# Kernel tuning notes

Hardware: AMD Instinct MI355X
Metric: run time of the kernel (lower is better)

## Reference

```python
import jax, jax.numpy as jnp
import numpy as np

D, H, NL, DFF, VS, VT = 512, 8, 6, 2048, 32000, 32000
B, SS, ST = 4, 512, 512
PAD = 1
EPS = 1e-5


def _pos_encoding(S, d):
    pos = jnp.arange(S, dtype=jnp.float32)[:, None]
    div = jnp.exp(jnp.arange(0, d, 2, dtype=jnp.float32) * (-jnp.log(jnp.float32(10000.0)) / d))
    pe = jnp.zeros((S, d), dtype=jnp.float32)
    pe = pe.at[:, 0::2].set(jnp.sin(pos * div))
    pe = pe.at[:, 1::2].set(jnp.cos(pos * div))
    return pe


def _ln(x, g, b):
    m = jnp.mean(x, axis=-1, keepdims=True)
    v = jnp.mean(jnp.square(x - m), axis=-1, keepdims=True)
    return (x - m) * jax.lax.rsqrt(v + EPS) * g + b


def _mha(q, k, v, Wq, Wk, Wv, Wo, mask):
    # q,k,v: [B,S,D]; W*: [D,D] (torch Linear: y = x @ W.T); mask True -> masked
    Bq, Sq, _ = q.shape
    Sk = k.shape[1]
    dk = D // H
    Q = (q @ Wq.T).reshape(Bq, Sq, H, dk).transpose(0, 2, 1, 3)
    K = (k @ Wk.T).reshape(Bq, Sk, H, dk).transpose(0, 2, 1, 3)
    V = (v @ Wv.T).reshape(Bq, Sk, H, dk).transpose(0, 2, 1, 3)
    scores = jnp.einsum('bhqd,bhkd->bhqk', Q, K) / jnp.sqrt(jnp.float32(dk))
    scores = jnp.where(mask, -jnp.inf, scores)
    w = jax.nn.softmax(scores, axis=-1)
    w = jnp.nan_to_num(w)  # matches torch.nan_to_num after softmax of all -inf rows
    out = jnp.einsum('bhqk,bhkd->bhqd', w, V)
    out = out.transpose(0, 2, 1, 3).reshape(Bq, Sq, D)
    return out @ Wo.T


def _ffn(x, w1, b1, w2, b2):
    return jax.nn.relu(x @ w1.T + b1) @ w2.T + b2


def setup_inputs() -> dict:
    key = jax.random.key(0)
    ks = jax.random.split(key, 48)
    i = iter(range(48))
    n = lambda shape, s=0.02: jax.random.normal(ks[next(i)], shape, dtype=jnp.float32) * s
    inp = {
        'src': jax.random.randint(ks[next(i)], (B, SS), 0, VS),
        'tgt': jax.random.randint(ks[next(i)], (B, ST), 0, VT),
        'src_embed': n((VS, D)),
        'tgt_embed': n((VT, D)),
        'enc_Wq': n((NL, D, D)), 'enc_Wk': n((NL, D, D)), 'enc_Wv': n((NL, D, D)), 'enc_Wo': n((NL, D, D)),
        'enc_w1': n((NL, DFF, D)), 'enc_b1': jnp.zeros((NL, DFF)),
        'enc_w2': n((NL, D, DFF)), 'enc_b2': jnp.zeros((NL, D)),
        'enc_ln1g': jnp.ones((NL, D)), 'enc_ln1b': jnp.zeros((NL, D)),
        'enc_ln2g': jnp.ones((NL, D)), 'enc_ln2b': jnp.zeros((NL, D)),
        'enc_lnfg': jnp.ones((D,)), 'enc_lnfb': jnp.zeros((D,)),
        'dec_sWq': n((NL, D, D)), 'dec_sWk': n((NL, D, D)), 'dec_sWv': n((NL, D, D)), 'dec_sWo': n((NL, D, D)),
        'dec_cWq': n((NL, D, D)), 'dec_cWk': n((NL, D, D)), 'dec_cWv': n((NL, D, D)), 'dec_cWo': n((NL, D, D)),
        'dec_w1': n((NL, DFF, D)), 'dec_b1': jnp.zeros((NL, DFF)),
        'dec_w2': n((NL, D, DFF)), 'dec_b2': jnp.zeros((NL, D)),
        'dec_ln1g': jnp.ones((NL, D)), 'dec_ln1b': jnp.zeros((NL, D)),
        'dec_ln2g': jnp.ones((NL, D)), 'dec_ln2b': jnp.zeros((NL, D)),
        'dec_ln3g': jnp.ones((NL, D)), 'dec_ln3b': jnp.zeros((NL, D)),
        'dec_lnfg': jnp.ones((D,)), 'dec_lnfb': jnp.zeros((D,)),
        'out_W': n((VT, D)), 'out_b': jnp.zeros((VT,)),
    }
    return inp


def reference(src, tgt, src_embed, tgt_embed,
              enc_Wq, enc_Wk, enc_Wv, enc_Wo, enc_w1, enc_b1, enc_w2, enc_b2,
              enc_ln1g, enc_ln1b, enc_ln2g, enc_ln2b, enc_lnfg, enc_lnfb,
              dec_sWq, dec_sWk, dec_sWv, dec_sWo, dec_cWq, dec_cWk, dec_cWv, dec_cWo,
              dec_w1, dec_b1, dec_w2, dec_b2,
              dec_ln1g, dec_ln1b, dec_ln2g, dec_ln2b, dec_ln3g, dec_ln3b,
              dec_lnfg, dec_lnfb, out_W, out_b):
    scale = jnp.sqrt(jnp.float32(D))
    src_mask = (src == PAD)[:, None, None, :]                      # [B,1,1,SS]
    causal = jnp.triu(jnp.ones((ST, ST), dtype=bool), k=1)[None, None]
    tgt_mask = (tgt == PAD)[:, None, None, :] | causal             # [B,1,ST,ST]

    # Encoder
    x = src_embed[src] * scale + _pos_encoding(SS, D)[None]
    for l in range(NL):
        nrm = _ln(x, enc_ln1g[l], enc_ln1b[l])
        x = x + _mha(nrm, nrm, nrm, enc_Wq[l], enc_Wk[l], enc_Wv[l], enc_Wo[l], src_mask)
        x = x + _ffn(_ln(x, enc_ln2g[l], enc_ln2b[l]), enc_w1[l], enc_b1[l], enc_w2[l], enc_b2[l])
    memory = _ln(x, enc_lnfg, enc_lnfb)

    # Decoder
    y = tgt_embed[tgt] * scale + _pos_encoding(ST, D)[None]
    for l in range(NL):
        nrm = _ln(y, dec_ln1g[l], dec_ln1b[l])
        y = y + _mha(nrm, nrm, nrm, dec_sWq[l], dec_sWk[l], dec_sWv[l], dec_sWo[l], tgt_mask)
        nrm = _ln(y, dec_ln2g[l], dec_ln2b[l])
        y = y + _mha(nrm, memory, memory, dec_cWq[l], dec_cWk[l], dec_cWv[l], dec_cWo[l], src_mask)
        y = y + _ffn(_ln(y, dec_ln3g[l], dec_ln3b[l]), dec_w1[l], dec_b1[l], dec_w2[l], dec_b2[l])
    y = _ln(y, dec_lnfg, dec_lnfb)

    logits = y @ out_W.T + out_b                                   # [B,ST,VT]
    return logits
```

## Files before the change

kernel.cpp:

```cpp
#include <hip/hip_runtime.h>
#include <hip/hip_bf16.h>
#include <math.h>

#define Dm    512
#define Hh    8
#define NLay  6
#define DFFm  2048
#define Bb    4
#define NTOK  2048
#define PADID 1
#define LNEPS 1e-5f
#define S2W   262144

typedef __attribute__((ext_vector_type(8))) short short8;
typedef __attribute__((ext_vector_type(4))) float f32x4;
typedef unsigned short u16;

__device__ __forceinline__ u16 f2bf(float f) {
    union { float f; unsigned int i; } x; x.f = f;
    unsigned int r = x.i + 0x7fffu + ((x.i >> 16) & 1u);
    return (u16)(r >> 16);
}

typedef const __attribute__((address_space(1))) void* as1cv;
typedef __attribute__((address_space(3))) void* as3v;
__device__ __forceinline__ void gl_lds16(const u16* g, u16* l) {
    __builtin_amdgcn_global_load_lds((as1cv)g, (as3v)l, 16, 0, 0);
}

__device__ __forceinline__ void swz_tile(int& mt, int& nt) {
    const int nwg  = gridDim.x * gridDim.y;
    const int orig = blockIdx.y * gridDim.x + blockIdx.x;
    const int q8 = nwg >> 3, r8 = nwg & 7;
    const int xcd = orig & 7, idx = orig >> 3;
    const int wgid = (xcd < r8 ? xcd * (q8 + 1) : r8 * (q8 + 1) + (xcd - r8) * q8) + idx;
    const int MT = gridDim.y;
    mt = wgid % MT;
    nt = wgid / MT;
}

struct CvtJobs {
    const float* s[17];
    u16*         d[17];
    long         n4[17];
};
__global__ __launch_bounds__(256) void cvt_many(CvtJobs j) {
    const int job = blockIdx.y;
    const long n4 = j.n4[job];
    const float* in = j.s[job];
    u16* out = j.d[job];
    long i = (long)blockIdx.x * 256 + threadIdx.x;
    const long stride = (long)gridDim.x * 256;
    for (; i < n4; i += stride) {
        float4 v = ((const float4*)in)[i];
        ushort4 o;
        o.x = f2bf(v.x); o.y = f2bf(v.y); o.z = f2bf(v.z); o.w = f2bf(v.w);
        ((ushort4*)out)[i] = o;
    }
}

__global__ __launch_bounds__(256) void gemm_bt(
    const u16* __restrict__ A, int lda,
    const u16* __restrict__ B0, const u16* __restrict__ B1,
    const u16* __restrict__ B2, int ldb,
    float* Cf, u16* Cb, int csm,
    const float* __restrict__ bias,
    const float* res, int ldres,
    int K, int vth, int koff, u16* vtp)
{
    __shared__ u16 As[2][4096];
    __shared__ u16 Bs[2][4096];
    int mt, nt; swz_tile(mt, nt);
    const int m0 = mt << 6, n0 = nt << 6;
    const int t = threadIdx.x, lane = t & 63, wave = t >> 6;
    const int wr = (wave >> 1) << 5, wc = (wave & 1) << 5;
    const int fr = lane & 15, fq = lane >> 4;
    const int srow = t >> 3;
    const int sch  = (t & 7) ^ (srow & 7);
    const u16* Bsel = (n0 < 512) ? B0 : (n0 < 1024 ? B1 : B2);
    const u16* Ag0 = A + (long)(m0 + srow) * lda + (sch << 3);
    const u16* Ag1 = A + (long)(m0 + 32 + srow) * lda + (sch << 3);
    const u16* Bg0 = Bsel + (long)((n0 & 511) + srow) * ldb + (sch << 3);
    const u16* Bg1 = Bsel + (long)((n0 & 511) + 32 + srow) * ldb + (sch << 3);

    f32x4 acc[2][2];
    #pragma unroll
    for (int i = 0; i < 2; i++)
        #pragma unroll
        for (int j = 0; j < 2; j++) acc[i][j] = (f32x4){0.f, 0.f, 0.f, 0.f};

    const int nk = K >> 6;
    gl_lds16(Ag0, &As[0][t << 3]);
    gl_lds16(Ag1, &As[0][(t + 256) << 3]);
    gl_lds16(Bg0, &Bs[0][t << 3]);
    gl_lds16(Bg1, &Bs[0][(t + 256) << 3]);
    __syncthreads();
    for (int ki = 0; ki < nk; ki++) {
        const int cur = ki & 1;
        if (ki + 1 < nk) {
            const int ko = (ki + 1) << 6;
            gl_lds16(Ag0 + ko, &As[cur ^ 1][t << 3]);
            gl_lds16(Ag1 + ko, &As[cur ^ 1][(t + 256) << 3]);
            gl_lds16(Bg0 + ko, &Bs[cur ^ 1][t << 3]);
            gl_lds16(Bg1 + ko, &Bs[cur ^ 1][(t + 256) << 3]);
        }
        const int r0 = wr + fr, r1 = wr + 16 + fr;
        const int c0 = wc + fr, c1 = wc + 16 + fr;
        #pragma unroll
        for (int h = 0; h < 2; h++) {
            const int lc = fq | (h << 2);
            short8 af0 = *(const short8*)&As[cur][(r0 << 6) + ((lc ^ (r0 & 7)) << 3)];
            short8 af1 = *(const short8*)&As[cur][(r1 << 6) + ((lc ^ (r1 & 7)) << 3)];
            short8 bf0 = *(const short8*)&Bs[cur][(c0 << 6) + ((lc ^ (c0 & 7)) << 3)];
            short8 bf1 = *(const short8*)&Bs[cur][(c1 << 6) + ((lc ^ (c1 & 7)) << 3)];
            acc[0][0] = __builtin_amdgcn_mfma_f32_16x16x32_bf16(af0, bf0, acc[0][0], 0, 0, 0);
            acc[0][1] = __builtin_amdgcn_mfma_f32_16x16x32_bf16(af0, bf1, acc[0][1], 0, 0, 0);
            acc[1][0] = __builtin_amdgcn_mfma_f32_16x16x32_bf16(af1, bf0, acc[1][0], 0, 0, 0);
            acc[1][1] = __builtin_amdgcn_mfma_f32_16x16x32_bf16(af1, bf1, acc[1][1], 0, 0, 0);
        }
        __syncthreads();
    }

    #pragma unroll
    for (int i = 0; i < 2; i++) {
        #pragma unroll
        for (int j = 0; j < 2; j++) {
            const int nl  = n0 + wc + (j << 4) + fr;
            const int mlb = m0 + wr + (i << 4) + (fq << 2);
            const float bsv = bias ? bias[nl] : 0.f;
            #pragma unroll
            for (int r = 0; r < 4; r++) {
                const int ml = mlb + r;
                float v = acc[i][j][r] + bsv;
                if (nl >= vth) {
                    vtp[(long)(ml >> 9) * S2W + (long)(nl - vth) * 512 + (ml & 511)] = f2bf(v);
                } else {
                    long ci = (long)ml * csm + nl + koff;
                    if (res) v += res[(long)ml * ldres + nl];
                    if (Cf) Cf[ci] = v;
                    if (Cb) Cb[ci] = f2bf(v);
                }
            }
        }
    }
}

__global__ __launch_bounds__(256) void gemm_big(
    const u16* __restrict__ A, int lda,
    const u16* __restrict__ B, int ldb,
    float* Cf, u16* Cb, int ldc,
    const float* __restrict__ bias, int relu, int K)
{
    __shared__ u16 As[2][4096];
    __shared__ u16 Bs[2][4096];
    int mt, nt; swz_tile(mt, nt);
    const int m0 = mt << 7, n0 = nt << 7;
    const int t = threadIdx.x, lane = t & 63, wave = t >> 6;
    const int wr = (wave >> 1) << 6, wc = (wave & 1) << 6;
    const int fr = lane & 15, fq = lane >> 4;
    const int srow = t >> 2;
    const int sch  = (t & 3) ^ ((srow >> 1) & 3);
    const u16* Ag0 = A + (long)(m0 + srow) * lda + (sch << 3);
    const u16* Ag1 = A + (long)(m0 + 64 + srow) * lda + (sch << 3);
    const u16* Bg0 = B + (long)(n0 + srow) * ldb + (sch << 3);
    const u16* Bg1 = B + (long)(n0 + 64 + srow) * ldb + (sch << 3);

    f32x4 acc[4][4];
    #pragma unroll
    for (int i = 0; i < 4; i++)
        #pragma unroll
        for (int j = 0; j < 4; j++) acc[i][j] = (f32x4){0.f, 0.f, 0.f, 0.f};

    const int nk = K >> 5;
    gl_lds16(Ag0, &As[0][t << 3]);
    gl_lds16(Ag1, &As[0][(t + 256) << 3]);
    gl_lds16(Bg0, &Bs[0][t << 3]);
    gl_lds16(Bg1, &Bs[0][(t + 256) << 3]);
    __syncthreads();
    for (int ki = 0; ki < nk; ki++) {
        const int cur = ki & 1;
        if (ki + 1 < nk) {
            const int ko = (ki + 1) << 5;
            gl_lds16(Ag0 + ko, &As[cur ^ 1][t << 3]);
            gl_lds16(Ag1 + ko, &As[cur ^ 1][(t + 256) << 3]);
            gl_lds16(Bg0 + ko, &Bs[cur ^ 1][t << 3]);
            gl_lds16(Bg1 + ko, &Bs[cur ^ 1][(t + 256) << 3]);
        }
        short8 af[4], bf[4];
        #pragma unroll
        for (int i = 0; i < 4; i++) {
            const int r = wr + (i << 4) + fr;
            af[i] = *(const short8*)&As[cur][(r << 5) + ((fq ^ ((r >> 1) & 3)) << 3)];
        }
        #pragma unroll
        for (int j = 0; j < 4; j++) {
            const int c = wc + (j << 4) + fr;
            bf[j] = *(const short8*)&Bs[cur][(c << 5) + ((fq ^ ((c >> 1) & 3)) << 3)];
        }
        #pragma unroll
        for (int i = 0; i < 4; i++)
            #pragma unroll
            for (int j = 0; j < 4; j++)
                acc[i][j] = __builtin_amdgcn_mfma_f32_16x16x32_bf16(af[i], bf[j], acc[i][j], 0, 0, 0);
        __syncthreads();
    }

    #pragma unroll
    for (int i = 0; i < 4; i++) {
        #pragma unroll
        for (int j = 0; j < 4; j++) {
            const int nl  = n0 + wc + (j << 4) + fr;
            const int mlb = m0 + wr + (i << 4) + (fq << 2);
            const float bsv = bias ? bias[nl] : 0.f;
            #pragma unroll
            for (int r = 0; r < 4; r++) {
                float v = acc[i][j][r] + bsv;
                if (relu) v = fmaxf(v, 0.f);
                long ci = (long)(mlb + r) * ldc + nl;
                if (Cf) Cf[ci] = v;
                if (Cb) Cb[ci] = f2bf(v);
            }
        }
    }
}

__global__ __launch_bounds__(256) void attn_fused(
    const u16* __restrict__ qkb, const u16* __restrict__ vt,
    const int* __restrict__ ids, u16* __restrict__ attc, int causal)
{
    __shared__ u16 Ks[2][4096];
    __shared__ u16 Vs[2][4096];
    __shared__ short Ps[4][16][72];
    const int t = threadIdx.x, lane = t & 63, w = t >> 6;
    const int fr = lane & 15, fq = lane >> 4;
    const int q0 = blockIdx.x << 6, h = blockIdx.y, b = blockIdx.z;

    const u16* qp = qkb + (long)(b * 512 + q0 + (w << 4) + fr) * 1024 + h * 64 + (fq << 3);
    short8 aq0 = *(const short8*)qp;
    short8 aq1 = *(const short8*)(qp + 32);

    const int sr = t >> 3, sc = (t & 7) ^ (sr & 7);
    const u16* kg0 = qkb + (long)(b * 512 + sr) * 1024 + 512 + h * 64 + (sc << 3);
    const u16* kg1 = kg0 + 32L * 1024;
    const u16* vg0 = vt + (long)b * S2W + (long)(h * 64 + sr) * 512 + (sc << 3);
    const u16* vg1 = vg0 + 32L * 512;

    unsigned pmask = 0;
    #pragma unroll
    for (int kt = 0; kt < 8; kt++)
        #pragma unroll
        for (int j = 0; j < 4; j++)
            if (ids[b * 512 + (kt << 6) + (j << 4) + fr] == PADID)
                pmask |= 1u << ((kt << 2) + j);

    float m[4], l[4]; f32x4 oc[4];
    #pragma unroll
    for (int r = 0; r < 4; r++) { m[r] = -INFINITY; l[r] = 0.f; oc[r] = (f32x4){0.f,0.f,0.f,0.f}; }

    const int lastkt = causal ? (q0 >> 6) : 7;
    auto stage = [&](int kt, int buf) {
        const long so = (long)(kt << 6);
        gl_lds16(kg0 + so * 1024, &Ks[buf][t << 3]);
        gl_lds16(kg1 + so * 1024, &Ks[buf][(t + 256) << 3]);
        gl_lds16(vg0 + so, &Vs[buf][t << 3]);
        gl_lds16(vg1 + so, &Vs[buf][(t + 256) << 3]);
    };
    stage(0, 0);
    __syncthreads();

    for (int kt = 0; kt <= lastkt; kt++) {
        const int cur = kt & 1;
        if (kt < lastkt) stage(kt + 1, cur ^ 1);

        f32x4 sc4[4];
        #pragma unroll
        for (int j = 0; j < 4; j++) sc4[j] = (f32x4){0.f,0.f,0.f,0.f};
        #pragma unroll
        for (int j = 0; j < 4; j++) {
            const int rr = (j << 4) + fr;
            short8 bk0 = *(const short8*)&Ks[cur][rr * 64 + ((fq ^ (rr & 7)) << 3)];
            short8 bk1 = *(const short8*)&Ks[cur][rr * 64 + (((fq | 4) ^ (rr & 7)) << 3)];
            sc4[j] = __builtin_amdgcn_mfma_f32_16x16x32_bf16(aq0, bk0, sc4[j], 0, 0, 0);
            sc4[j] = __builtin_amdgcn_mfma_f32_16x16x32_bf16(aq1, bk1, sc4[j], 0, 0, 0);
        }
        const int s0 = kt << 6;
        #pragma unroll
        for (int r = 0; r < 4; r++) {
            const int qa = q0 + (w << 4) + (fq << 2) + r;
            float mx = -INFINITY;
            #pragma unroll
            for (int j = 0; j < 4; j++) {
                bool msk = ((pmask >> ((kt << 2) + j)) & 1) ||
                           (causal && (s0 + (j << 4) + fr) > qa);
                float sv = msk ? -INFINITY : sc4[j][r] * 0.125f;
                sc4[j][r] = sv;
                mx = fmaxf(mx, sv);
            }
            mx = fmaxf(mx, __shfl_xor(mx, 1)); mx = fmaxf(mx, __shfl_xor(mx, 2));
            mx = fmaxf(mx, __shfl_xor(mx, 4)); mx = fmaxf(mx, __shfl_xor(mx, 8));
            float mnew  = fmaxf(m[r], mx);
            float scale = (mnew == -INFINITY) ? 1.f : __expf(m[r] - mnew);
            float ps = 0.f;
            #pragma unroll
            for (int j = 0; j < 4; j++) {
                float p = (sc4[j][r] == -INFINITY) ? 0.f : __expf(sc4[j][r] - mnew);
                sc4[j][r] = p; ps += p;
            }
            ps += __shfl_xor(ps, 1); ps += __shfl_xor(ps, 2);
            ps += __shfl_xor(ps, 4); ps += __shfl_xor(ps, 8);
            l[r] = l[r] * scale + ps;
            m[r] = mnew;
            #pragma unroll
            for (int j2 = 0; j2 < 4; j2++) oc[j2][r] *= scale;
        }
        #pragma unroll
        for (int r = 0; r < 4; r++)
            #pragma unroll
            for (int j = 0; j < 4; j++)
                Ps[w][(fq << 2) + r][(j << 4) + fr] = (short)f2bf(sc4[j][r]);
        #pragma unroll
        for (int kc = 0; kc < 2; kc++) {
            short8 pa = *(const short8*)&Ps[w][fr][(kc << 5) + (fq << 3)];
            #pragma unroll
            for (int j2 = 0; j2 < 4; j2++) {
                const int rd = (j2 << 4) + fr;
                const int cch = (((kc << 2) | fq) ^ (rd & 7));
                short8 bv = *(const short8*)&Vs[cur][rd * 64 + (cch << 3)];
                oc[j2] = __builtin_amdgcn_mfma_f32_16x16x32_bf16(pa, bv, oc[j2], 0, 0, 0);
            }
        }
        __syncthreads();
    }

    float inv[4];
    #pragma unroll
    for (int r = 0; r < 4; r++) inv[r] = (l[r] > 0.f) ? 1.f / l[r] : 0.f;
    #pragma unroll
    for (int j2 = 0; j2 < 4; j2++)
        #pragma unroll
        for (int r = 0; r < 4; r++)
            attc[(long)(b * 512 + q0 + (w << 4) + (fq << 2) + r) * 512 + h * 64 + (j2 << 4) + fr]
                = f2bf(oc[j2][r] * inv[r]);
}

__global__ __launch_bounds__(256) void ln_rows(
    const float* __restrict__ x, const float* __restrict__ g,
    const float* __restrict__ b, u16* __restrict__ out)
{
    int row  = blockIdx.x * 4 + (threadIdx.x >> 6);
    int lane = threadIdx.x & 63;
    const float* xr = x + (long)row * Dm;
    float v[8]; float s = 0.f;
    #pragma unroll
    for (int i = 0; i < 8; i++) { v[i] = xr[lane + (i << 6)]; s += v[i]; }
    #pragma unroll
    for (int o = 32; o > 0; o >>= 1) s += __shfl_xor(s, o);
    float mean = s * (1.f / 512.f);
    float q = 0.f;
    #pragma unroll
    for (int i = 0; i < 8; i++) { float d = v[i] - mean; q += d * d; }
    #pragma unroll
    for (int o = 32; o > 0; o >>= 1) q += __shfl_xor(q, o);
    float rinv = rsqrtf(q * (1.f / 512.f) + LNEPS);
    u16* orow = out + (long)row * Dm;
    #pragma unroll
    for (int i = 0; i < 8; i++) {
        int c = lane + (i << 6);
        orow[c] = f2bf((v[i] - mean) * rinv * g[c] + b[c]);
    }
}

__global__ __launch_bounds__(256) void embed_pe(
    const int* __restrict__ ids, const float* __restrict__ emb,
    float* __restrict__ out)
{
    int idx = blockIdx.x * 256 + threadIdx.x;
    int d   = idx & 511;
    int tok = idx >> 9;
    int s   = tok & 511;
    int id  = ids[tok];
    float val = emb[(long)id * Dm + d] * 22.62741699796952f;
    int i2 = d >> 1;
    float dv  = expf((float)(i2 << 1) * (-9.210340371976184f / 512.f));
    float ang = (float)s * dv;
    val += (d & 1) ? cosf(ang) : sinf(ang);
    out[idx] = val;
}

extern "C" void kernel_launch(void* const* d_in, const int* in_sizes, int n_in,
                              void* d_out, int out_size, void* d_ws, size_t ws_size,
                              hipStream_t stream)
{
    (void)in_sizes; (void)n_in; (void)out_size; (void)ws_size;
    const int*   src       = (const int*)d_in[0];
    const int*   tgt       = (const int*)d_in[1];
    const float* src_embed = (const float*)d_in[2];
    const float* tgt_embed = (const float*)d_in[3];
    const float* enc_b1  = (const float*)d_in[9];
    const float* enc_b2  = (const float*)d_in[11];
    const float* enc_ln1g = (const float*)d_in[12];
    const float* enc_ln1b = (const float*)d_in[13];
    const float* enc_ln2g = (const float*)d_in[14];
    const float* enc_ln2b = (const float*)d_in[15];
    const float* enc_lnfg = (const float*)d_in[16];
    const float* enc_lnfb = (const float*)d_in[17];
    const float* dec_b1  = (const float*)d_in[27];
    const float* dec_b2  = (const float*)d_in[29];
    const float* dec_ln1g = (const float*)d_in[30];
    const float* dec_ln1b = (const float*)d_in[31];
    const float* dec_ln2g = (const float*)d_in[32];
    const float* dec_ln2b = (const float*)d_in[33];
    const float* dec_ln3g = (const float*)d_in[34];
    const float* dec_ln3b = (const float*)d_in[35];
    const float* dec_lnfg = (const float*)d_in[36];
    const float* dec_lnfb = (const float*)d_in[37];
    const float* out_b  = (const float*)d_in[39];

    char* wp = (char*)d_ws;
    auto carve = [&](size_t nbytes) {
        void* p = (void*)wp; wp += (nbytes + 255) & ~(size_t)255; return p;
    };

    const long nW = (long)NLay * S2W;
    const long nF = (long)NLay * DFFm * Dm;
    const long nO = 32000L * Dm;

    u16* Wb[12];
    for (int i = 0; i < 12; i++) Wb[i] = (u16*)carve((size_t)nW * 2);
    u16* w1E  = (u16*)carve((size_t)nF * 2);
    u16* w2E  = (u16*)carve((size_t)nF * 2);
    u16* w1D  = (u16*)carve((size_t)nF * 2);
    u16* w2D  = (u16*)carve((size_t)nF * 2);
    u16* outW = (u16*)carve((size_t)nO * 2);

    float* x  = (float*)carve((size_t)NTOK * Dm * 4);
    float* y  = (float*)carve((size_t)NTOK * Dm * 4);
    u16* nrm  = (u16*)carve((size_t)NTOK * Dm * 2);
    u16* qkb  = (u16*)carve((size_t)NTOK * 1024 * 2);
    u16* vt   = (u16*)carve((size_t)Bb * Dm * 512 * 2);
    u16* attc = (u16*)carve((size_t)NTOK * Dm * 2);
    u16* h1   = (u16*)carve((size_t)NTOK * DFFm * 2);
    u16* memn = (u16*)carve((size_t)NTOK * Dm * 2);

    const int wi[12] = {4, 5, 6, 7, 18, 19, 20, 21, 22, 23, 24, 25};
    CvtJobs jobs;
    for (int i = 0; i < 12; i++) {
        jobs.s[i] = (const float*)d_in[wi[i]]; jobs.d[i] = Wb[i]; jobs.n4[i] = nW >> 2;
    }
    jobs.s[12] = (const float*)d_in[8];  jobs.d[12] = w1E;  jobs.n4[12] = nF >> 2;
    jobs.s[13] = (const float*)d_in[10]; jobs.d[13] = w2E;  jobs.n4[13] = nF >> 2;
    jobs.s[14] = (const float*)d_in[26]; jobs.d[14] = w1D;  jobs.n4[14] = nF >> 2;
    jobs.s[15] = (const float*)d_in[28]; jobs.d[15] = w2D;  jobs.n4[15] = nF >> 2;
    jobs.s[16] = (const float*)d_in[38]; jobs.d[16] = outW; jobs.n4[16] = nO >> 2;
    cvt_many<<<dim3(512, 17), 256, 0, stream>>>(jobs);

    const int BIG = 1 << 28;
    u16 *eWq = Wb[0], *eWk = Wb[1], *eWv = Wb[2], *eWo = Wb[3];
    u16 *sWq = Wb[4], *sWk = Wb[5], *sWv = Wb[6], *sWo = Wb[7];
    u16 *cWq = Wb[8], *cWk = Wb[9], *cWv = Wb[10], *cWo = Wb[11];

    embed_pe<<<4096, 256, 0, stream>>>(src, src_embed, x);
    for (int l = 0; l < NLay; l++) {
        const size_t wo = (size_t)l * S2W;
        ln_rows<<<512, 256, 0, stream>>>(x, enc_ln1g + l * Dm, enc_ln1b + l * Dm, nrm);
        gemm_bt<<<dim3(24, 32), 256, 0, stream>>>(nrm, 512, eWq + wo, eWk + wo, eWv + wo, 512,
            nullptr, qkb, 1024, nullptr, nullptr, 0, 512, 1024, 0, vt);
        attn_fused<<<dim3(8, Hh, Bb), 256, 0, stream>>>(qkb, vt, src, attc, 0);
        gemm_bt<<<dim3(8, 32), 256, 0, stream>>>(attc, 512, eWo + wo, nullptr, nullptr, 512,
            x, nullptr, 512, nullptr, x, 512, 512, BIG, 0, nullptr);
        ln_rows<<<512, 256, 0, stream>>>(x, enc_ln2g + l * Dm, enc_ln2b + l * Dm, nrm);
        gemm_big<<<dim3(16, 16), 256, 0, stream>>>(nrm, 512, w1E + (size_t)l * DFFm * Dm, 512,
            nullptr, h1, DFFm, enc_b1 + l * DFFm, 1, 512);
        gemm_bt<<<dim3(8, 32), 256, 0, stream>>>(h1, DFFm, w2E + (size_t)l * Dm * DFFm,
            nullptr, nullptr, DFFm, x, nullptr, 512, enc_b2 + l * Dm, x, 512, 2048, BIG, 0, nullptr);
    }
    ln_rows<<<512, 256, 0, stream>>>(x, enc_lnfg, enc_lnfb, memn);

    embed_pe<<<4096, 256, 0, stream>>>(tgt, tgt_embed, y);
    for (int l = 0; l < NLay; l++) {
        const size_t wo = (size_t)l * S2W;
        ln_rows<<<512, 256, 0, stream>>>(y, dec_ln1g + l * Dm, dec_ln1b + l * Dm, nrm);
        gemm_bt<<<dim3(24, 32), 256, 0, stream>>>(nrm, 512, sWq + wo, sWk + wo, sWv + wo, 512,
            nullptr, qkb, 1024, nullptr, nullptr, 0, 512, 1024, 0, vt);
        attn_fused<<<dim3(8, Hh, Bb), 256, 0, stream>>>(qkb, vt, tgt, attc, 1);
        gemm_bt<<<dim3(8, 32), 256, 0, stream>>>(attc, 512, sWo + wo, nullptr, nullptr, 512,
            y, nullptr, 512, nullptr, y, 512, 512, BIG, 0, nullptr);
        ln_rows<<<512, 256, 0, stream>>>(y, dec_ln2g + l * Dm, dec_ln2b + l * Dm, nrm);
        gemm_bt<<<dim3(8, 32), 256, 0, stream>>>(nrm, 512, cWq + wo, nullptr, nullptr, 512,
            nullptr, qkb, 1024, nullptr, nullptr, 0, 512, BIG, 0, nullptr);
        gemm_bt<<<dim3(16, 32), 256, 0, stream>>>(memn, 512, cWk + wo, cWv + wo, nullptr, 512,
            nullptr, qkb, 1024, nullptr, nullptr, 0, 512, 512, 512, vt);
        attn_fused<<<dim3(8, Hh, Bb), 256, 0, stream>>>(qkb, vt, src, attc, 0);
        gemm_bt<<<dim3(8, 32), 256, 0, stream>>>(attc, 512, cWo + wo, nullptr, nullptr, 512,
            y, nullptr, 512, nullptr, y, 512, 512, BIG, 0, nullptr);
        ln_rows<<<512, 256, 0, stream>>>(y, dec_ln3g + l * Dm, dec_ln3b + l * Dm, nrm);
        gemm_big<<<dim3(16, 16), 256, 0, stream>>>(nrm, 512, w1D + (size_t)l * DFFm * Dm, 512,
            nullptr, h1, DFFm, dec_b1 + l * DFFm, 1, 512);
        gemm_bt<<<dim3(8, 32), 256, 0, stream>>>(h1, DFFm, w2D + (size_t)l * Dm * DFFm,
            nullptr, nullptr, DFFm, y, nullptr, 512, dec_b2 + l * Dm, y, 512, 2048, BIG, 0, nullptr);
    }
    ln_rows<<<512, 256, 0, stream>>>(y, dec_lnfg, dec_lnfb, nrm);

    gemm_big<<<dim3(250, 16), 256, 0, stream>>>(nrm, 512, outW, 512,
        (float*)d_out, nullptr, 32000, out_b, 0, 512);
}
```

Baseline: 1.857 ms.

## Fuse LayerNorm into GEMM prologue, split-K atomic residual GEMMs, retile vocab GEMM

Result: slower. 3.617 ms (+94.8%).

```diff
diff --git a/kernel.cpp b/kernel.cpp
--- a/kernel.cpp
+++ b/kernel.cpp
@@ -59,14 +59,134 @@
     }
 }
 
+__global__ __launch_bounds__(256) void gemm_lnbt(
+    const float* __restrict__ X0, const float* __restrict__ X1,
+    const float* __restrict__ g0p, const float* __restrict__ b0p,
+    const float* __restrict__ g1p, const float* __restrict__ b1p,
+    const u16* __restrict__ B0, const u16* __restrict__ B1,
+    const u16* __restrict__ B2,
+    u16* __restrict__ Cb, int csm,
+    const float* __restrict__ bias, int relu,
+    int vth, u16* vtp)
+{
+    extern __shared__ u16 lds[];
+    u16* As  = lds;
+    u16* Bs0 = lds + 64 * 512;
+    u16* Bs1 = Bs0 + 4096;
+    int mt, nt; swz_tile(mt, nt);
+    const int m0 = mt << 6, n0 = nt << 6;
+    const int t = threadIdx.x, lane = t & 63, wave = t >> 6;
+
+    const int p = B1 ? (n0 >> 9) : 0;
+    const float* X  = p ? X1 : X0;
+    const float* gp = p ? g1p : g0p;
+    const float* bp = p ? b1p : b0p;
+    const u16* Bmat; int nb;
+    if (B1) { Bmat = (p == 0) ? B0 : (p == 1 ? B1 : B2); nb = n0 & 511; }
+    else    { Bmat = B0; nb = n0; }
+
+    const int rr = t >> 2, qq = t & 3;
+    const float* xr = X + (long)(m0 + rr) * 512 + (qq << 7);
+    float s = 0.f, ss = 0.f;
+    #pragma unroll
+    for (int i = 0; i < 32; i++) {
+        float4 v = ((const float4*)xr)[i];
+        s  += v.x + v.y + v.z + v.w;
+        ss += v.x * v.x + v.y * v.y + v.z * v.z + v.w * v.w;
+    }
+    s  += __shfl_xor(s, 1);  s  += __shfl_xor(s, 2);
+    ss += __shfl_xor(ss, 1); ss += __shfl_xor(ss, 2);
+    const float mean = s * (1.f / 512.f);
+    const float rstd = rsqrtf(fmaxf(ss * (1.f / 512.f) - mean * mean, 0.f) + LNEPS);
+    #pragma unroll
+    for (int i = 0; i < 32; i += 2) {
+        float4 a = ((const float4*)xr)[i];
+        float4 c = ((const float4*)xr)[i + 1];
+        const int k0 = (qq << 7) + (i << 2);
+        float4 ga = *(const float4*)&gp[k0], gc = *(const float4*)&gp[k0 + 4];
+        float4 ba = *(const float4*)&bp[k0], bc = *(const float4*)&bp[k0 + 4];
+        short8 o;
+        o[0] = (short)f2bf((a.x - mean) * rstd * ga.x + ba.x);
+        o[1] = (short)f2bf((a.y - mean) * rstd * ga.y + ba.y);
+        o[2] = (short)f2bf((a.z - mean) * rstd * ga.z + ba.z);
+        o[3] = (short)f2bf((a.w - mean) * rstd * ga.w + ba.w);
+        o[4] = (short)f2bf((c.x - mean) * rstd * gc.x + bc.x);
+        o[5] = (short)f2bf((c.y - mean) * rstd * gc.y + bc.y);
+        o[6] = (short)f2bf((c.z - mean) * rstd * gc.z + bc.z);
+        o[7] = (short)f2bf((c.w - mean) * rstd * gc.w + bc.w);
+        const int ch = k0 >> 3;
+        *(short8*)&As[(rr << 9) + ((ch ^ (rr & 7)) << 3)] = o;
+    }
+
+    const int sr = t >> 3, sc = (t & 7) ^ (sr & 7);
+    const u16* Bg0 = Bmat + (long)(nb + sr) * 512 + (sc << 3);
+    const u16* Bg1 = Bg0 + 32L * 512;
+    gl_lds16(Bg0, Bs0 + (t << 3));
+    gl_lds16(Bg1, Bs0 + ((t + 256) << 3));
+    __syncthreads();
+
+    const int wr = (wave >> 1) << 5, wc = (wave & 1) << 5;
+    const int fr = lane & 15, fq = lane >> 4;
+    f32x4 acc[2][2];
+    #pragma unroll
+    for (int i = 0; i < 2; i++)
+        #pragma unroll
+        for (int j = 0; j < 2; j++) acc[i][j] = (f32x4){0.f, 0.f, 0.f, 0.f};
+
+    for (int ki = 0; ki < 8; ki++) {
+        u16* Bc = (ki & 1) ? Bs1 : Bs0;
+        u16* Bn = (ki & 1) ? Bs0 : Bs1;
+        if (ki + 1 < 8) {
+            const int ko = (ki + 1) << 6;
+            gl_lds16(Bg0 + ko, Bn + (t << 3));
+            gl_lds16(Bg1 + ko, Bn + ((t + 256) << 3));
+        }
+        const int r0 = wr + fr, r1 = wr + 16 + fr;
+        const int c0 = wc + fr, c1 = wc + 16 + fr;
+        #pragma unroll
+        for (int h = 0; h < 2; h++) {
+            const int lc = fq | (h << 2);
+            const int gA = (ki << 3) | lc;
+            short8 af0 = *(const short8*)&As[(r0 << 9) + ((gA ^ (r0 & 7)) << 3)];
+            short8 af1 = *(const short8*)&As[(r1 << 9) + ((gA ^ (r1 & 7)) << 3)];
+            short8 bf0 = *(const short8*)&Bc[(c0 << 6) + ((lc ^ (c0 & 7)) << 3)];
+            short8 bf1 = *(const short8*)&Bc[(c1 << 6) + ((lc ^ (c1 & 7)) << 3)];
+            acc[0][0] = __builtin_amdgcn_mfma_f32_16x16x32_bf16(af0, bf0, acc[0][0], 0, 0, 0);
+            acc[0][1] = __builtin_amdgcn_mfma_f32_16x16x32_bf16(af0, bf1, acc[0][1], 0, 0, 0);
+            acc[1][0] = __builtin_amdgcn_mfma_f32_16x16x32_bf16(af1, bf0, acc[1][0], 0, 0, 0);
+            acc[1][1] = __builtin_amdgcn_mfma_f32_16x16x32_bf16(af1, bf1, acc[1][1], 0, 0, 0);
+        }
+        __syncthreads();
+    }
+
+    #pragma unroll
+    for (int i = 0; i < 2; i++) {
+        #pragma unroll
+        for (int j = 0; j < 2; j++) {
+            const int nl  = n0 + wc + (j << 4) + fr;
+            const int mlb = m0 + wr + (i << 4) + (fq << 2);
+            const float bsv = bias ? bias[nl] : 0.f;
+            #pragma unroll
+            for (int r = 0; r < 4; r++) {
+                const int ml = mlb + r;
+                float v = acc[i][j][r] + bsv;
+                if (nl >= vth) {
+                    vtp[(long)(ml >> 9) * S2W + (long)(nl - vth) * 512 + (ml & 511)] = f2bf(v);
+                } else {
+                    if (relu) v = fmaxf(v, 0.f);
+                    Cb[(long)ml * csm + nl] = f2bf(v);
+                }
+            }
+        }
+    }
+}
+
 __global__ __launch_bounds__(256) void gemm_bt(
-    const u16* __restrict__ A, int lda,
-    const u16* __restrict__ B0, const u16* __restrict__ B1,
-    const u16* __restrict__ B2, int ldb,
-    float* Cf, u16* Cb, int csm,
+    const u16* __restrict__ A0, int lda,
+    const u16* __restrict__ B0, int ldb,
+    float* Cf, int csm,
     const float* __restrict__ bias,
-    const float* res, int ldres,
-    int K, int vth, int koff, u16* vtp)
+    int Kc, int ns)
 {
     __shared__ u16 As[2][4096];
     __shared__ u16 Bs[2][4096];
@@ -77,11 +197,12 @@
     const int fr = lane & 15, fq = lane >> 4;
     const int srow = t >> 3;
     const int sch  = (t & 7) ^ (srow & 7);
-    const u16* Bsel = (n0 < 512) ? B0 : (n0 < 1024 ? B1 : B2);
-    const u16* Ag0 = A + (long)(m0 + srow) * lda + (sch << 3);
-    const u16* Ag1 = A + (long)(m0 + 32 + srow) * lda + (sch << 3);
-    const u16* Bg0 = Bsel + (long)((n0 & 511) + srow) * ldb + (sch << 3);
-    const u16* Bg1 = Bsel + (long)((n0 & 511) + 32 + srow) * ldb + (sch << 3);
+    const long kb = (long)blockIdx.z * Kc;
+
+    const u16* Ag0 = A0 + (long)(m0 + srow) * lda + kb + (sch << 3);
+    const u16* Ag1 = Ag0 + 32L * lda;
+    const u16* Bg0 = B0 + (long)(n0 + srow) * ldb + kb + (sch << 3);
+    const u16* Bg1 = Bg0 + 32L * ldb;
 
     f32x4 acc[2][2];
     #pragma unroll
@@ -89,7 +210,7 @@
         #pragma unroll
         for (int j = 0; j < 2; j++) acc[i][j] = (f32x4){0.f, 0.f, 0.f, 0.f};
 
-    const int nk = K >> 6;
+    const int nk = Kc >> 6;
     gl_lds16(Ag0, &As[0][t << 3]);
     gl_lds16(Ag1, &As[0][(t + 256) << 3]);
     gl_lds16(Bg0, &Bs[0][t << 3]);
@@ -127,19 +248,13 @@
         for (int j = 0; j < 2; j++) {
             const int nl  = n0 + wc + (j << 4) + fr;
             const int mlb = m0 + wr + (i << 4) + (fq << 2);
-            const float bsv = bias ? bias[nl] : 0.f;
+            const float bsv = (bias && blockIdx.z == 0) ? bias[nl] : 0.f;
             #pragma unroll
             for (int r = 0; r < 4; r++) {
                 const int ml = mlb + r;
                 float v = acc[i][j][r] + bsv;
-                if (nl >= vth) {
-                    vtp[(long)(ml >> 9) * S2W + (long)(nl - vth) * 512 + (ml & 511)] = f2bf(v);
-                } else {
-                    long ci = (long)ml * csm + nl + koff;
-                    if (res) v += res[(long)ml * ldres + nl];
-                    if (Cf) Cf[ci] = v;
-                    if (Cb) Cb[ci] = f2bf(v);
-                }
+                if (ns > 1) unsafeAtomicAdd(&Cf[(long)ml * csm + nl], v);
+                else        Cf[(long)ml * csm + nl] = v;
             }
         }
     }
@@ -148,22 +263,29 @@
 __global__ __launch_bounds__(256) void gemm_big(
     const u16* __restrict__ A, int lda,
     const u16* __restrict__ B, int ldb,
-    float* Cf, u16* Cb, int ldc,
-    const float* __restrict__ bias, int relu, int K)
+    float* Cf, int ldc,
+    const float* __restrict__ bias, int K)
 {
-    __shared__ u16 As[2][4096];
-    __shared__ u16 Bs[2][4096];
+    extern __shared__ u16 lds[];
+    u16* As0 = lds;
+    u16* As1 = lds + 8192;
+    u16* Bs0 = lds + 16384;
+    u16* Bs1 = lds + 24576;
     int mt, nt; swz_tile(mt, nt);
     const int m0 = mt << 7, n0 = nt << 7;
     const int t = threadIdx.x, lane = t & 63, wave = t >> 6;
     const int wr = (wave >> 1) << 6, wc = (wave & 1) << 6;
     const int fr = lane & 15, fq = lane >> 4;
-    const int srow = t >> 2;
-    const int sch  = (t & 3) ^ ((srow >> 1) & 3);
-    const u16* Ag0 = A + (long)(m0 + srow) * lda + (sch << 3);
-    const u16* Ag1 = A + (long)(m0 + 64 + srow) * lda + (sch << 3);
-    const u16* Bg0 = B + (long)(n0 + srow) * ldb + (sch << 3);
-    const u16* Bg1 = B + (long)(n0 + 64 + srow) * ldb + (sch << 3);
+    const int sr = t >> 3;
+    const int sc = (t & 7) ^ (sr & 7);
+    const u16* Ag0 = A + (long)(m0 + sr) * lda + (sc << 3);
+    const u16* Ag1 = Ag0 + 32L * lda;
+    const u16* Ag2 = Ag0 + 64L * lda;
+    const u16* Ag3 = Ag0 + 96L * lda;
+    const u16* Bg0 = B + (long)(n0 + sr) * ldb + (sc << 3);
+    const u16* Bg1 = Bg0 + 32L * ldb;
+    const u16* Bg2 = Bg0 + 64L * ldb;
+    const u16* Bg3 = Bg0 + 96L * ldb;
 
     f32x4 acc[4][4];
     #pragma unroll
@@ -171,37 +293,54 @@
         #pragma unroll
         for (int j = 0; j < 4; j++) acc[i][j] = (f32x4){0.f, 0.f, 0.f, 0.f};
 
-    const int nk = K >> 5;
-    gl_lds16(Ag0, &As[0][t << 3]);
-    gl_lds16(Ag1, &As[0][(t + 256) << 3]);
-    gl_lds16(Bg0, &Bs[0][t << 3]);
-    gl_lds16(Bg1, &Bs[0][(t + 256) << 3]);
+    const int nk = K >> 6;
+    {
+        gl_lds16(Ag0, As0 + (t << 3));
+        gl_lds16(Ag1, As0 + ((t + 256) << 3));
+        gl_lds16(Ag2, As0 + ((t + 512) << 3));
+        gl_lds16(Ag3, As0 + ((t + 768) << 3));
+        gl_lds16(Bg0, Bs0 + (t << 3));
+        gl_lds16(Bg1, Bs0 + ((t + 256) << 3));
+        gl_lds16(Bg2, Bs0 + ((t + 512) << 3));
+        gl_lds16(Bg3, Bs0 + ((t + 768) << 3));
+    }
     __syncthreads();
     for (int ki = 0; ki < nk; ki++) {
-        const int cur = ki & 1;
+        u16* Ac = (ki & 1) ? As1 : As0;
+        u16* Bc = (ki & 1) ? Bs1 : Bs0;
+        u16* An = (ki & 1) ? As0 : As1;
+        u16* Bn = (ki & 1) ? Bs0 : Bs1;
         if (ki + 1 < nk) {
-            const int ko = (ki + 1) << 5;
-            gl_lds16(Ag0 + ko, &As[cur ^ 1][t << 3]);
-            gl_lds16(Ag1 + ko, &As[cur ^ 1][(t + 256) << 3]);
-            gl_lds16(Bg0 + ko, &Bs[cur ^ 1][t << 3]);
-            gl_lds16(Bg1 + ko, &Bs[cur ^ 1][(t + 256) << 3]);
-        }
-        short8 af[4], bf[4];
-        #pragma unroll
-        for (int i = 0; i < 4; i++) {
-            const int r = wr + (i << 4) + fr;
-            af[i] = *(const short8*)&As[cur][(r << 5) + ((fq ^ ((r >> 1) & 3)) << 3)];
-        }
-        #pragma unroll
-        for (int j = 0; j < 4; j++) {
-            const int c = wc + (j << 4) + fr;
-            bf[j] = *(const short8*)&Bs[cur][(c << 5) + ((fq ^ ((c >> 1) & 3)) << 3)];
-        }
-        #pragma unroll
-        for (int i = 0; i < 4; i++)
-            #pragma unroll
-            for (int j = 0; j < 4; j++)
-                acc[i][j] = __builtin_amdgcn_mfma_f32_16x16x32_bf16(af[i], bf[j], acc[i][j], 0, 0, 0);
+            const int ko = (ki + 1) << 6;
+            gl_lds16(Ag0 + ko, An + (t << 3));
+            gl_lds16(Ag1 + ko, An + ((t + 256) << 3));
+            gl_lds16(Ag2 + ko, An + ((t + 512) << 3));
+            gl_lds16(Ag3 + ko, An + ((t + 768) << 3));
+            gl_lds16(Bg0 + ko, Bn + (t << 3));
+            gl_lds16(Bg1 + ko, Bn + ((t + 256) << 3));
+            gl_lds16(Bg2 + ko, Bn + ((t + 512) << 3));
+            gl_lds16(Bg3 + ko, Bn + ((t + 768) << 3));
+        }
+        #pragma unroll
+        for (int h = 0; h < 2; h++) {
+            const int lc = fq | (h << 2);
+            short8 af[4], bf[4];
+            #pragma unroll
+            for (int i = 0; i < 4; i++) {
+                const int r = wr + (i << 4) + fr;
+                af[i] = *(const short8*)&Ac[(r << 6) + ((lc ^ (r & 7)) << 3)];
+            }
+            #pragma unroll
+            for (int j = 0; j < 4; j++) {
+                const int c = wc + (j << 4) + fr;
+                bf[j] = *(const short8*)&Bc[(c << 6) + ((lc ^ (c & 7)) << 3)];
+            }
+            #pragma unroll
+            for (int i = 0; i < 4; i++)
+                #pragma unroll
+                for (int j = 0; j < 4; j++)
+                    acc[i][j] = __builtin_amdgcn_mfma_f32_16x16x32_bf16(af[i], bf[j], acc[i][j], 0, 0, 0);
+        }
         __syncthreads();
     }
 
@@ -213,13 +352,8 @@
             const int mlb = m0 + wr + (i << 4) + (fq << 2);
             const float bsv = bias ? bias[nl] : 0.f;
             #pragma unroll
-            for (int r = 0; r < 4; r++) {
-                float v = acc[i][j][r] + bsv;
-                if (relu) v = fmaxf(v, 0.f);
-                long ci = (long)(mlb + r) * ldc + nl;
-                if (Cf) Cf[ci] = v;
-                if (Cb) Cb[ci] = f2bf(v);
-            }
+            for (int r = 0; r < 4; r++)
+                Cf[(long)(mlb + r) * ldc + nl] = acc[i][j][r] + bsv;
         }
     }
 }
@@ -440,7 +574,6 @@
     u16* vt   = (u16*)carve((size_t)Bb * Dm * 512 * 2);
     u16* attc = (u16*)carve((size_t)NTOK * Dm * 2);
     u16* h1   = (u16*)carve((size_t)NTOK * DFFm * 2);
-    u16* memn = (u16*)carve((size_t)NTOK * Dm * 2);
 
     const int wi[12] = {4, 5, 6, 7, 18, 19, 20, 21, 22, 23, 24, 25};
     CvtJobs jobs;
@@ -459,48 +592,50 @@
     u16 *sWq = Wb[4], *sWk = Wb[5], *sWv = Wb[6], *sWo = Wb[7];
     u16 *cWq = Wb[8], *cWk = Wb[9], *cWv = Wb[10], *cWo = Wb[11];
 
+    const size_t LNB = 64 * 512 * 2 + 2 * 4096 * 2;
+    const size_t BGB = 4 * 8192 * 2;
+
     embed_pe<<<4096, 256, 0, stream>>>(src, src_embed, x);
     for (int l = 0; l < NLay; l++) {
         const size_t wo = (size_t)l * S2W;
-        ln_rows<<<512, 256, 0, stream>>>(x, enc_ln1g + l * Dm, enc_ln1b + l * Dm, nrm);
-        gemm_bt<<<dim3(24, 32), 256, 0, stream>>>(nrm, 512, eWq + wo, eWk + wo, eWv + wo, 512,
-            nullptr, qkb, 1024, nullptr, nullptr, 0, 512, 1024, 0, vt);
+        gemm_lnbt<<<dim3(24, 32), 256, LNB, stream>>>(
+            x, x, enc_ln1g + l * Dm, enc_ln1b + l * Dm, enc_ln1g + l * Dm, enc_ln1b + l * Dm,
+            eWq + wo, eWk + wo, eWv + wo, qkb, 1024, nullptr, 0, 1024, vt);
         attn_fused<<<dim3(8, Hh, Bb), 256, 0, stream>>>(qkb, vt, src, attc, 0);
-        gemm_bt<<<dim3(8, 32), 256, 0, stream>>>(attc, 512, eWo + wo, nullptr, nullptr, 512,
-            x, nullptr, 512, nullptr, x, 512, 512, BIG, 0, nullptr);
-        ln_rows<<<512, 256, 0, stream>>>(x, enc_ln2g + l * Dm, enc_ln2b + l * Dm, nrm);
-        gemm_big<<<dim3(16, 16), 256, 0, stream>>>(nrm, 512, w1E + (size_t)l * DFFm * Dm, 512,
-            nullptr, h1, DFFm, enc_b1 + l * DFFm, 1, 512);
-        gemm_bt<<<dim3(8, 32), 256, 0, stream>>>(h1, DFFm, w2E + (size_t)l * Dm * DFFm,
-            nullptr, nullptr, DFFm, x, nullptr, 512, enc_b2 + l * Dm, x, 512, 2048, BIG, 0, nullptr);
-    }
-    ln_rows<<<512, 256, 0, stream>>>(x, enc_lnfg, enc_lnfb, memn);
+        gemm_bt<<<dim3(8, 32, 2), 256, 0, stream>>>(attc, 512, eWo + wo, 512,
+            x, 512, nullptr, 256, 2);
+        gemm_lnbt<<<dim3(32, 32), 256, LNB, stream>>>(
+            x, x, enc_ln2g + l * Dm, enc_ln2b + l * Dm, enc_ln2g + l * Dm, enc_ln2b + l * Dm,
+            w1E + (size_t)l * DFFm * Dm, nullptr, nullptr, h1, DFFm,
+            enc_b1 + l * DFFm, 1, BIG, nullptr);
+        gemm_bt<<<dim3(8, 32, 4), 256, 0, stream>>>(h1, DFFm, w2E + (size_t)l * Dm * DFFm, DFFm,
+            x, 512, enc_b2 + l * Dm, 512, 4);
+    }
 
     embed_pe<<<4096, 256, 0, stream>>>(tgt, tgt_embed, y);
     for (int l = 0; l < NLay; l++) {
         const size_t wo = (size_t)l * S2W;
-        ln_rows<<<512, 256, 0, stream>>>(y, dec_ln1g + l * Dm, dec_ln1b + l * Dm, nrm);
-        gemm_bt<<<dim3(24, 32), 256, 0, stream>>>(nrm, 512, sWq + wo, sWk + wo, sWv + wo, 512,
-            nullptr, qkb, 1024, nullptr, nullptr, 0, 512, 1024, 0, vt);
+        gemm_lnbt<<<dim3(24, 32), 256, LNB, stream>>>(
+            y, y, dec_ln1g + l * Dm, dec_ln1b + l * Dm, dec_ln1g + l * Dm, dec_ln1b + l * Dm,
+            sWq + wo, sWk + wo, sWv + wo, qkb, 1024, nullptr, 0, 1024, vt);
         attn_fused<<<dim3(8, Hh, Bb), 256, 0, stream>>>(qkb, vt, tgt, attc, 1);
-        gemm_bt<<<dim3(8, 32), 256, 0, stream>>>(attc, 512, sWo + wo, nullptr, nullptr, 512,
-            y, nullptr, 512, nullptr, y, 512, 512, BIG, 0, nullptr);
-        ln_rows<<<512, 256, 0, stream>>>(y, dec_ln2g + l * Dm, dec_ln2b + l * Dm, nrm);
-        gemm_bt<<<dim3(8, 32), 256, 0, stream>>>(nrm, 512, cWq + wo, nullptr, nullptr, 512,
-            nullptr, qkb, 1024, nullptr, nullptr, 0, 512, BIG, 0, nullptr);
-        gemm_bt<<<dim3(16, 32), 256, 0, stream>>>(memn, 512, cWk + wo, cWv + wo, nullptr, 512,
-            nullptr, qkb, 1024, nullptr, nullptr, 0, 512, 512, 512, vt);
+        gemm_bt<<<dim3(8, 32, 2), 256, 0, stream>>>(attc, 512, sWo + wo, 512,
+            y, 512, nullptr, 256, 2);
+        gemm_lnbt<<<dim3(24, 32), 256, LNB, stream>>>(
+            y, x, dec_ln2g + l * Dm, dec_ln2b + l * Dm, enc_lnfg, enc_lnfb,
+            cWq + wo, cWk + wo, cWv + wo, qkb, 1024, nullptr, 0, 1024, vt);
         attn_fused<<<dim3(8, Hh, Bb), 256, 0, stream>>>(qkb, vt, src, attc, 0);
-        gemm_bt<<<dim3(8, 32), 256, 0, stream>>>(attc, 512, cWo + wo, nullptr, nullptr, 512,
-            y, nullptr, 512, nullptr, y, 512, 512, BIG, 0, nullptr);
-        ln_rows<<<512, 256, 0, stream>>>(y, dec_ln3g + l * Dm, dec_ln3b + l * Dm, nrm);
-        gemm_big<<<dim3(16, 16), 256, 0, stream>>>(nrm, 512, w1D + (size_t)l * DFFm * Dm, 512,
-            nullptr, h1, DFFm, dec_b1 + l * DFFm, 1, 512);
-        gemm_bt<<<dim3(8, 32), 256, 0, stream>>>(h1, DFFm, w2D + (size_t)l * Dm * DFFm,
-            nullptr, nullptr, DFFm, y, nullptr, 512, dec_b2 + l * Dm, y, 512, 2048, BIG, 0, nullptr);
+        gemm_bt<<<dim3(8, 32, 2), 256, 0, stream>>>(attc, 512, cWo + wo, 512,
+            y, 512, nullptr, 256, 2);
+        gemm_lnbt<<<dim3(32, 32), 256, LNB, stream>>>(
+            y, y, dec_ln3g + l * Dm, dec_ln3b + l * Dm, dec_ln3g + l * Dm, dec_ln3b + l * Dm,
+            w1D + (size_t)l * DFFm * Dm, nullptr, nullptr, h1, DFFm,
+            dec_b1 + l * DFFm, 1, BIG, nullptr);
+        gemm_bt<<<dim3(8, 32, 4), 256, 0, stream>>>(h1, DFFm, w2D + (size_t)l * Dm * DFFm, DFFm,
+            y, 512, dec_b2 + l * Dm, 512, 4);
     }
     ln_rows<<<512, 256, 0, stream>>>(y, dec_lnfg, dec_lnfb, nrm);
 
-    gemm_big<<<dim3(250, 16), 256, 0, stream>>>(nrm, 512, outW, 512,
-        (float*)d_out, nullptr, 32000, out_b, 0, 512);
-}
+    gemm_big<<<dim3(250, 16), 256, BGB, stream>>>(nrm, 512, outW, 512,
+        (float*)d_out, 32000, out_b, 512);
+}
```
